# Kernel tuning notes

Hardware: AMD Instinct MI355X
Metric: run time of the kernel (lower is better)

The kernel has to match this reference:

```python
import jax, jax.numpy as jnp
import numpy as np

N = 100000       # nodes
E = 1600000      # edges (avg degree 16)
D_IN = 128
D_HID = 32
D_OUT = 32
H = 4            # heads
NEG_SLOPE = 0.2  # GATConv default leaky_relu slope


def setup_inputs() -> dict:
    key = jax.random.key(0)
    ks = jax.random.split(key, 10)
    s = 0.1
    return {
        "edge": jax.random.randint(ks[0], (2, E), 0, N),
        "features": jax.random.normal(ks[1], (N, D_IN), jnp.float32),
        # layer 1 params: W [in, H*hid], attention vectors per head [H, hid]
        "W1": jax.random.normal(ks[2], (D_IN, H * D_HID), jnp.float32) * s,
        "a1_src": jax.random.normal(ks[3], (H, D_HID), jnp.float32) * s,
        "a1_dst": jax.random.normal(ks[4], (H, D_HID), jnp.float32) * s,
        "b1": jnp.zeros((H * D_HID,), jnp.float32),
        # layer 2 params
        "W2": jax.random.normal(ks[5], (H * D_HID, H * D_OUT), jnp.float32) * s,
        "a2_src": jax.random.normal(ks[6], (H, D_OUT), jnp.float32) * s,
        "a2_dst": jax.random.normal(ks[7], (H, D_OUT), jnp.float32) * s,
        "b2": jnp.zeros((H * D_OUT,), jnp.float32),
    }


def gat_conv(x, src, dst, W, a_src, a_dst, b, heads, d_out):
    """Multi-head GAT layer, concat heads. x: [N, d_in] -> [N, heads*d_out]."""
    n = x.shape[0]
    h = (x @ W).reshape(n, heads, d_out)                 # [N,H,D]
    e_src = jnp.einsum('nhd,hd->nh', h, a_src)           # [N,H]
    e_dst = jnp.einsum('nhd,hd->nh', h, a_dst)           # [N,H]
    e = jax.nn.leaky_relu(e_src[src] + e_dst[dst], NEG_SLOPE)  # [E,H]
    # softmax over incoming edges of each dst node (stable via segment max)
    m = jax.lax.stop_gradient(jax.ops.segment_max(e, dst, num_segments=n))
    w = jnp.exp(e - m[dst])                              # [E,H]
    den = jax.ops.segment_sum(w, dst, num_segments=n)    # [N,H]
    alpha = w / den[dst]                                 # [E,H]
    out = jax.ops.segment_sum(alpha[:, :, None] * h[src], dst, num_segments=n)
    return out.reshape(n, heads * d_out) + b


def reference(edge, features, W1, a1_src, a1_dst, b1, W2, a2_src, a2_dst, b2):
    src, dst = edge[0], edge[1]
    h = jax.nn.relu(gat_conv(features, src, dst, W1, a1_src, a1_dst, b1, H, D_HID))
    h = gat_conv(h, src, dst, W2, a2_src, a2_dst, b2, H, D_OUT)
    return jax.nn.log_softmax(h, axis=1)
```

## Files before the change

kernel.cpp:

```cpp
#include <hip/hip_runtime.h>
#include <hip/hip_bf16.h>
#include <math.h>

#define N_NODES 100000
#define N_EDGES 1600000
#define NHEADS 4
#define NEG_SLOPE 0.2f
#define NB 1563
#define BCAP 2048

typedef __attribute__((ext_vector_type(8))) short short8;
typedef __attribute__((ext_vector_type(4))) float f32x4;

__device__ __forceinline__ unsigned short f2bf(float f) {
    unsigned int u = __float_as_uint(f);
    u += 0x7fffu + ((u >> 16) & 1u);
    return (unsigned short)(u >> 16);
}
__device__ __forceinline__ float bf_lo(unsigned int u) {
    return __uint_as_float(u << 16);
}
__device__ __forceinline__ float bf_hi(unsigned int u) {
    return __uint_as_float(u & 0xffff0000u);
}
__device__ __forceinline__ short8 pack8(float4 f0, float4 f1) {
    short8 v;
    v[0] = (short)f2bf(f0.x); v[1] = (short)f2bf(f0.y);
    v[2] = (short)f2bf(f0.z); v[3] = (short)f2bf(f0.w);
    v[4] = (short)f2bf(f1.x); v[5] = (short)f2bf(f1.y);
    v[6] = (short)f2bf(f1.z); v[7] = (short)f2bf(f1.w);
    return v;
}

__global__ void pack_w_kernel(const float* __restrict__ W,
                              const float* __restrict__ a_src,
                              const float* __restrict__ a_dst,
                              unsigned short* __restrict__ Wp) {
    int idx = blockIdx.x * 256 + threadIdx.x;
    if (idx >= 18432) return;
    int j    = idx & 7;
    int lane = (idx >> 3) & 63;
    int kc   = (idx >> 9) & 3;
    int ct   = idx >> 11;
    int k = kc * 32 + ((lane >> 4) & 3) * 8 + j;
    int n = lane & 15;
    float v = 0.f;
    if (ct < 8) {
        v = W[k * 128 + ct * 16 + n];
    } else if (n < 8) {
        int hd = n & 3;
        const float* av = (n < 4 ? a_src : a_dst) + hd * 32;
        const float* wr = W + k * 128 + hd * 32;
#pragma unroll
        for (int t = 0; t < 32; ++t) v = fmaf(wr[t], av[t], v);
    }
    Wp[idx] = f2bf(v);
}

template <bool XF32>
__global__ __launch_bounds__(256) void gemm_mfma_kernel(
        const void* __restrict__ xv,
        const unsigned short* __restrict__ Wp,
        unsigned short* __restrict__ h, float* __restrict__ esd, int n_rows) {
    __shared__ unsigned short Wl[18432];

    const int t = threadIdx.x;
    {
        const uint4* s4 = (const uint4*)Wp;
        uint4* d4 = (uint4*)Wl;
#pragma unroll
        for (int p = 0; p < 9; ++p) d4[p * 256 + t] = s4[p * 256 + t];
    }
    __syncthreads();

    const int lane = t & 63, wave = t >> 6;
    const int l15 = lane & 15, quad = lane >> 4;
    const int rbase = blockIdx.x * 128 + wave * 32;

    short8 a[2][4];
#pragma unroll
    for (int rt = 0; rt < 2; ++rt) {
        int r = rbase + rt * 16 + l15;
        r = r < n_rows ? r : n_rows - 1;
        if (XF32) {
            const float* xr = (const float*)xv + (size_t)r * 128 + quad * 8;
#pragma unroll
            for (int kc = 0; kc < 4; ++kc) {
                float4 f0 = *(const float4*)(xr + kc * 32);
                float4 f1 = *(const float4*)(xr + kc * 32 + 4);
                a[rt][kc] = pack8(f0, f1);
            }
        } else {
            const unsigned short* xr =
                (const unsigned short*)xv + (size_t)r * 128 + quad * 8;
#pragma unroll
            for (int kc = 0; kc < 4; ++kc)
                a[rt][kc] = *(const short8*)(xr + kc * 32);
        }
    }

    f32x4 acc[2][9];
#pragma unroll
    for (int rt = 0; rt < 2; ++rt)
#pragma unroll
        for (int ct = 0; ct < 9; ++ct)
            acc[rt][ct] = (f32x4){0.f, 0.f, 0.f, 0.f};

#pragma unroll
    for (int ct = 0; ct < 9; ++ct) {
#pragma unroll
        for (int kc = 0; kc < 4; ++kc) {
            short8 b = *(const short8*)&Wl[((ct * 4 + kc) * 64 + lane) * 8];
            acc[0][ct] = __builtin_amdgcn_mfma_f32_16x16x32_bf16(
                a[0][kc], b, acc[0][ct], 0, 0, 0);
            acc[1][ct] = __builtin_amdgcn_mfma_f32_16x16x32_bf16(
                a[1][kc], b, acc[1][ct], 0, 0, 0);
        }
    }

#pragma unroll
    for (int rt = 0; rt < 2; ++rt) {
#pragma unroll
        for (int i = 0; i < 4; ++i) {
            int r = rbase + rt * 16 + quad * 4 + i;
            if (r < n_rows) {
                unsigned short* hp = h + (size_t)r * 128 + l15;
#pragma unroll
                for (int ct = 0; ct < 8; ++ct)
                    hp[ct * 16] = f2bf(acc[rt][ct][i]);
                if (l15 < 8) esd[r * 8 + l15] = acc[rt][8][i];
            }
        }
    }
}

__global__ void zero_ints_kernel(int* __restrict__ p, int n) {
    int i = blockIdx.x * 256 + threadIdx.x;
    if (i < n) p[i] = 0;
}

__global__ void bucket_fill_kernel(const int* __restrict__ src,
                                   const int* __restrict__ dst,
                                   int* __restrict__ bcnt,
                                   unsigned int* __restrict__ slab) {
    int e = blockIdx.x * 256 + threadIdx.x;
    if (e >= N_EDGES) return;
    int d = dst[e];
    int b = d >> 6;
    int pos = atomicAdd(&bcnt[b * 16], 1);
    slab[(size_t)b * BCAP + pos] = (unsigned int)src[e] | ((unsigned int)(d & 63) << 17);
}

__global__ __launch_bounds__(256) void bucket_hist_kernel(
        const int* __restrict__ bcnt, const unsigned int* __restrict__ slab,
        int* __restrict__ deg) {
    __shared__ int hist[64];
    const int b = blockIdx.x;
    if (threadIdx.x < 64) hist[threadIdx.x] = 0;
    __syncthreads();
    const int m = bcnt[b * 16];
    const unsigned int* sp = slab + (size_t)b * BCAP;
    for (int i = threadIdx.x; i < m; i += 256)
        atomicAdd(&hist[sp[i] >> 17], 1);
    __syncthreads();
    if (threadIdx.x < 64) {
        int node = b * 64 + threadIdx.x;
        if (node < N_NODES) deg[node] = hist[threadIdx.x];
    }
}

__global__ __launch_bounds__(256) void scan1_kernel(const int* __restrict__ deg,
                                                    int* __restrict__ rowptr,
                                                    int* __restrict__ partials) {
    __shared__ int wsum[4];
    int i = blockIdx.x * 256 + threadIdx.x;
    int lane = threadIdx.x & 63, wave = threadIdx.x >> 6;
    int orig = (i < N_NODES) ? deg[i] : 0;
    int v = orig;
#pragma unroll
    for (int off = 1; off < 64; off <<= 1) {
        int t = __shfl_up(v, off);
        if (lane >= off) v += t;
    }
    if (lane == 63) wsum[wave] = v;
    __syncthreads();
    int woff = 0;
#pragma unroll
    for (int w = 0; w < 4; ++w) if (w < wave) woff += wsum[w];
    if (i < N_NODES) rowptr[i] = v - orig + woff;
    if (threadIdx.x == 0)
        partials[blockIdx.x] = wsum[0] + wsum[1] + wsum[2] + wsum[3];
}

__global__ __launch_bounds__(512) void scan2_kernel(int* __restrict__ partials,
                                                    int nb) {
    __shared__ int wsum[8];
    int i = threadIdx.x;
    int lane = i & 63, wave = i >> 6;
    int orig = (i < nb) ? partials[i] : 0;
    int v = orig;
#pragma unroll
    for (int off = 1; off < 64; off <<= 1) {
        int t = __shfl_up(v, off);
        if (lane >= off) v += t;
    }
    if (lane == 63) wsum[wave] = v;
    __syncthreads();
    int woff = 0;
#pragma unroll
    for (int w = 0; w < 8; ++w) if (w < wave) woff += wsum[w];
    if (i < nb) partials[i] = v - orig + woff;
}

__global__ void scan3_kernel(int* __restrict__ rowptr,
                             const int* __restrict__ partials) {
    int i = blockIdx.x * 256 + threadIdx.x;
    if (i < N_NODES) rowptr[i] += partials[blockIdx.x];
}

__global__ __launch_bounds__(256) void bucket_scatter_kernel(
        const int* __restrict__ bcnt, const unsigned int* __restrict__ slab,
        const int* __restrict__ rowptr, int* __restrict__ csr_src) {
    __shared__ int rp[64];
    __shared__ int cnt[64];
    const int b = blockIdx.x;
    if (threadIdx.x < 64) {
        int node = b * 64 + threadIdx.x;
        rp[threadIdx.x] = node < N_NODES ? rowptr[node] : 0;
        cnt[threadIdx.x] = 0;
    }
    __syncthreads();
    const int m = bcnt[b * 16];
    const unsigned int* sp = slab + (size_t)b * BCAP;
    for (int i = threadIdx.x; i < m; i += 256) {
        unsigned int rec = sp[i];
        int local = rec >> 17;
        int pos = rp[local] + atomicAdd(&cnt[local], 1);
        csr_src[pos] = (int)(rec & 0x1FFFFu);
    }
}

template <bool LOGSOFTMAX>
__global__ __launch_bounds__(256) void aggregate_kernel(
        const int* __restrict__ csr_src, const int* __restrict__ rowptr,
        const int* __restrict__ deg, const float* __restrict__ esd,
        const unsigned short* __restrict__ hb, const float* __restrict__ b,
        void* __restrict__ out) {
    const int lane = threadIdx.x & 63;
    const int wave = threadIdx.x >> 6;
    const int n = blockIdx.x * 4 + wave;
    if (n >= N_NODES) return;
    const int eo = lane >> 4;
    const int cl = lane & 15;
    const int c0 = cl * 8;
    const int hd = cl >> 2;
    const float edn = esd[n * 8 + 4 + hd];
    const int base = rowptr[n];
    const int dg = deg[n];

    float acc[8] = {0.f, 0.f, 0.f, 0.f, 0.f, 0.f, 0.f, 0.f};
    float wsum = 0.f;

    if (dg > 0) {
        const int myidx = csr_src[base + (lane < dg ? lane : dg - 1)];
        const int nit = (dg + 3) >> 2;

        auto getS = [&](int j) -> int {
            int o = 4 * j + eo;
            if (4 * j < 64) return __shfl(myidx, o);
            int oc = o < dg ? o : dg - 1;
            return csr_src[base + oc];
        };
        auto loadP = [&](int s) -> uint4 {
            return *(const uint4*)(hb + (size_t)s * 128 + c0);
        };

        int s0 = getS(0);
        uint4 p0 = loadP(s0);
        float e0 = esd[s0 * 8 + hd];
        uint4 p1 = p0; float e1 = e0;
        if (nit > 1) {
            int s1 = getS(1);
            p1 = loadP(s1);
            e1 = esd[s1 * 8 + hd];
        }
        for (int j = 0; j < nit; ++j) {
            uint4 p2 = p1; float e2 = e1;
            if (j + 2 < nit) {
                int s2 = getS(j + 2);
                p2 = loadP(s2);
                e2 = esd[s2 * 8 + hd];
            }
            int o = 4 * j + eo;
            float sc = e0 + edn;
            sc = sc > 0.f ? sc : NEG_SLOPE * sc;
            float w = (o < dg) ? __expf(sc) : 0.f;
            acc[0] = fmaf(w, bf_lo(p0.x), acc[0]);
            acc[1] = fmaf(w, bf_hi(p0.x), acc[1]);
            acc[2] = fmaf(w, bf_lo(p0.y), acc[2]);
            acc[3] = fmaf(w, bf_hi(p0.y), acc[3]);
            acc[4] = fmaf(w, bf_lo(p0.z), acc[4]);
            acc[5] = fmaf(w, bf_hi(p0.z), acc[5]);
            acc[6] = fmaf(w, bf_lo(p0.w), acc[6]);
            acc[7] = fmaf(w, bf_hi(p0.w), acc[7]);
            wsum += w;
            p0 = p1; e0 = e1; p1 = p2; e1 = e2;
        }
    }

#pragma unroll
    for (int j = 0; j < 8; ++j) {
        acc[j] += __shfl_xor(acc[j], 16);
        acc[j] += __shfl_xor(acc[j], 32);
    }
    wsum += __shfl_xor(wsum, 16);
    wsum += __shfl_xor(wsum, 32);

    float inv = wsum > 0.f ? 1.f / wsum : 0.f;
    float bl[8];
    *(float4*)&bl[0] = *(const float4*)(b + c0);
    *(float4*)&bl[4] = *(const float4*)(b + c0 + 4);
    float v[8];
#pragma unroll
    for (int j = 0; j < 8; ++j) v[j] = acc[j] * inv + bl[j];

    if (!LOGSOFTMAX) {
        if (lane < 16) {
            unsigned int pk[4];
#pragma unroll
            for (int j = 0; j < 4; ++j) {
                float r0 = v[2 * j]     > 0.f ? v[2 * j]     : 0.f;
                float r1 = v[2 * j + 1] > 0.f ? v[2 * j + 1] : 0.f;
                pk[j] = (unsigned int)f2bf(r0) | ((unsigned int)f2bf(r1) << 16);
            }
            *(uint4*)((unsigned short*)out + (size_t)n * 128 + c0) =
                make_uint4(pk[0], pk[1], pk[2], pk[3]);
        }
    } else {
        float m = v[0];
#pragma unroll
        for (int j = 1; j < 8; ++j) m = fmaxf(m, v[j]);
#pragma unroll
        for (int s = 1; s < 16; s <<= 1) m = fmaxf(m, __shfl_xor(m, s));
        float se = 0.f;
#pragma unroll
        for (int j = 0; j < 8; ++j) se += __expf(v[j] - m);
#pragma unroll
        for (int s = 1; s < 16; s <<= 1) se += __shfl_xor(se, s);
        float ls = m + logf(se);
        if (lane < 16) {
            float* o = (float*)out + (size_t)n * 128 + c0;
            *(float4*)o = make_float4(v[0] - ls, v[1] - ls, v[2] - ls, v[3] - ls);
            *(float4*)(o + 4) = make_float4(v[4] - ls, v[5] - ls, v[6] - ls, v[7] - ls);
        }
    }
}

extern "C" void kernel_launch(void* const* d_in, const int* in_sizes, int n_in,
                              void* d_out, int out_size, void* d_ws, size_t ws_size,
                              hipStream_t stream) {
    const int*   edge = (const int*)d_in[0];
    const int*   src  = edge;
    const int*   dst  = edge + N_EDGES;
    const float* feat = (const float*)d_in[1];
    const float* W1   = (const float*)d_in[2];
    const float* a1s  = (const float*)d_in[3];
    const float* a1d  = (const float*)d_in[4];
    const float* b1   = (const float*)d_in[5];
    const float* W2   = (const float*)d_in[6];
    const float* a2s  = (const float*)d_in[7];
    const float* a2d  = (const float*)d_in[8];
    const float* b2   = (const float*)d_in[9];
    float* out = (float*)d_out;

    unsigned short* hb  = (unsigned short*)d_ws;
    unsigned short* x1b = hb + (size_t)N_NODES * 128;
    unsigned short* Wp1 = x1b + (size_t)N_NODES * 128;
    unsigned short* Wp2 = Wp1 + 18432;
    float* esd = (float*)(Wp2 + 18432);
    int* deg      = (int*)(esd + (size_t)N_NODES * 8);
    int* rowptr   = deg + N_NODES;
    int* partials = rowptr + N_NODES;
    int* bcnt     = partials + 512;
    unsigned int* slab = (unsigned int*)(bcnt + NB * 16);
    int* csr_src  = (int*)(slab + (size_t)NB * BCAP);

    const int node_blk  = (N_NODES + 255) / 256;
    const int edge_blk  = (N_EDGES + 255) / 256;
    const int gemm_blk  = (N_NODES + 127) / 128;
    const int agg_blk   = (N_NODES + 3) / 4;

    zero_ints_kernel<<<(NB * 16 + 255) / 256, 256, 0, stream>>>(bcnt, NB * 16);
    bucket_fill_kernel<<<edge_blk, 256, 0, stream>>>(src, dst, bcnt, slab);
    bucket_hist_kernel<<<NB, 256, 0, stream>>>(bcnt, slab, deg);
    scan1_kernel<<<node_blk, 256, 0, stream>>>(deg, rowptr, partials);
    scan2_kernel<<<1, 512, 0, stream>>>(partials, node_blk);
    scan3_kernel<<<node_blk, 256, 0, stream>>>(rowptr, partials);
    bucket_scatter_kernel<<<NB, 256, 0, stream>>>(bcnt, slab, rowptr, csr_src);

    pack_w_kernel<<<72, 256, 0, stream>>>(W1, a1s, a1d, Wp1);
    pack_w_kernel<<<72, 256, 0, stream>>>(W2, a2s, a2d, Wp2);

    gemm_mfma_kernel<true><<<gemm_blk, 256, 0, stream>>>(feat, Wp1, hb, esd, N_NODES);
    aggregate_kernel<false><<<agg_blk, 256, 0, stream>>>(
        csr_src, rowptr, deg, esd, hb, b1, x1b);

    gemm_mfma_kernel<false><<<gemm_blk, 256, 0, stream>>>(x1b, Wp2, hb, esd, N_NODES);
    aggregate_kernel<true><<<agg_blk, 256, 0, stream>>>(
        csr_src, rowptr, deg, esd, hb, b2, out);
}
```

Baseline: 401.9 us.

## Two-level binning for CSR build and batched gathers in aggregation

Replaces per-edge global atomics into 1563 small buckets with a block-local shared-memory binning into 49 coarse buckets split into 8 sub-slabs, flushed to global memory in 16-element chunks. Histogram and scatter then work on 2048-node buckets with larger shared arrays. The aggregate kernel issues up to 8 neighbour row loads up front instead of a depth-2 software pipeline. It also splits the src and dst attention scores into separate arrays so each source score is loaded by one lane and shuffled to the others. The trade-offs are fixed capacities (SUBCAP, BUKCAP) that could overflow on skewed degree distributions, and higher register use in aggregation.

After: 410.7 us. 1.02x slower.

```diff
diff --git a/kernel.cpp b/kernel.cpp
--- a/kernel.cpp
+++ b/kernel.cpp
@@ -6,8 +6,9 @@
 #define N_EDGES 1600000
 #define NHEADS 4
 #define NEG_SLOPE 0.2f
-#define NB 1563
-#define BCAP 2048
+#define NBUK 49
+#define BUKCAP 272
+#define SUBCAP 4608
 
 typedef __attribute__((ext_vector_type(8))) short short8;
 typedef __attribute__((ext_vector_type(4))) float f32x4;
@@ -61,7 +62,8 @@
 __global__ __launch_bounds__(256) void gemm_mfma_kernel(
         const void* __restrict__ xv,
         const unsigned short* __restrict__ Wp,
-        unsigned short* __restrict__ h, float* __restrict__ esd, int n_rows) {
+        unsigned short* __restrict__ h,
+        float* __restrict__ es, float* __restrict__ ed, int n_rows) {
     __shared__ unsigned short Wl[18432];
 
     const int t = threadIdx.x;
@@ -128,7 +130,8 @@
 #pragma unroll
                 for (int ct = 0; ct < 8; ++ct)
                     hp[ct * 16] = f2bf(acc[rt][ct][i]);
-                if (l15 < 8) esd[r * 8 + l15] = acc[rt][8][i];
+                if (l15 < 4)      es[r * 4 + l15]       = acc[rt][8][i];
+                else if (l15 < 8) ed[r * 4 + (l15 - 4)] = acc[rt][8][i];
             }
         }
     }
@@ -139,33 +142,75 @@
     if (i < n) p[i] = 0;
 }
 
-__global__ void bucket_fill_kernel(const int* __restrict__ src,
-                                   const int* __restrict__ dst,
-                                   int* __restrict__ bcnt,
-                                   unsigned int* __restrict__ slab) {
-    int e = blockIdx.x * 256 + threadIdx.x;
-    if (e >= N_EDGES) return;
-    int d = dst[e];
-    int b = d >> 6;
-    int pos = atomicAdd(&bcnt[b * 16], 1);
-    slab[(size_t)b * BCAP + pos] = (unsigned int)src[e] | ((unsigned int)(d & 63) << 17);
-}
-
-__global__ __launch_bounds__(256) void bucket_hist_kernel(
-        const int* __restrict__ bcnt, const unsigned int* __restrict__ slab,
+__global__ __launch_bounds__(256) void bin_fill_kernel(
+        const int* __restrict__ src, const int* __restrict__ dst,
+        int* __restrict__ gcnt, unsigned int* __restrict__ slab) {
+    __shared__ unsigned int lbuf[NBUK * BUKCAP];
+    __shared__ int cnt[NBUK];
+    const int t = threadIdx.x;
+    const int sub = blockIdx.x & 7;
+    if (t < NBUK) cnt[t] = 0;
+    __syncthreads();
+
+    const int per = (N_EDGES + gridDim.x - 1) / gridDim.x;
+    const int e0 = blockIdx.x * per;
+    const int e1 = (e0 + per < N_EDGES) ? e0 + per : N_EDGES;
+
+    for (int eb = e0; eb < e1; eb += 256) {
+        int e = eb + t;
+        if (e < e1) {
+            int d = dst[e];
+            int s = src[e];
+            int bk = d >> 11;
+            int pos = atomicAdd(&cnt[bk], 1);
+            lbuf[bk * BUKCAP + pos] =
+                (unsigned int)s | ((unsigned int)(d & 2047) << 17);
+        }
+        __syncthreads();
+        if (t < NBUK) {
+            int pending = cnt[t];
+            int nl = pending >> 4;
+            if (nl > 0) {
+                int gpos = atomicAdd(&gcnt[(t * 8 + sub) * 16], nl * 16);
+                unsigned int* gp =
+                    slab + (size_t)(t * 8 + sub) * SUBCAP + gpos;
+                for (int l = 0; l < nl * 16; l += 4)
+                    *(uint4*)(gp + l) = *(uint4*)&lbuf[t * BUKCAP + l];
+                int rem = pending & 15;
+                for (int r2 = 0; r2 < rem; ++r2)
+                    lbuf[t * BUKCAP + r2] = lbuf[t * BUKCAP + nl * 16 + r2];
+                cnt[t] = rem;
+            }
+        }
+        __syncthreads();
+    }
+    if (t < NBUK) {
+        int rem = cnt[t];
+        if (rem > 0) {
+            int gpos = atomicAdd(&gcnt[(t * 8 + sub) * 16], rem);
+            unsigned int* gp = slab + (size_t)(t * 8 + sub) * SUBCAP + gpos;
+            for (int r2 = 0; r2 < rem; ++r2) gp[r2] = lbuf[t * BUKCAP + r2];
+        }
+    }
+}
+
+__global__ __launch_bounds__(256) void bin_hist_kernel(
+        const int* __restrict__ gcnt, const unsigned int* __restrict__ slab,
         int* __restrict__ deg) {
-    __shared__ int hist[64];
+    __shared__ int hist[2048];
+    const int t = threadIdx.x;
     const int b = blockIdx.x;
-    if (threadIdx.x < 64) hist[threadIdx.x] = 0;
-    __syncthreads();
-    const int m = bcnt[b * 16];
-    const unsigned int* sp = slab + (size_t)b * BCAP;
-    for (int i = threadIdx.x; i < m; i += 256)
-        atomicAdd(&hist[sp[i] >> 17], 1);
-    __syncthreads();
-    if (threadIdx.x < 64) {
-        int node = b * 64 + threadIdx.x;
-        if (node < N_NODES) deg[node] = hist[threadIdx.x];
+    for (int i = t; i < 2048; i += 256) hist[i] = 0;
+    __syncthreads();
+    for (int sub = 0; sub < 8; ++sub) {
+        int m = gcnt[(b * 8 + sub) * 16];
+        const unsigned int* sp = slab + (size_t)(b * 8 + sub) * SUBCAP;
+        for (int i = t; i < m; i += 256) atomicAdd(&hist[sp[i] >> 17], 1);
+    }
+    __syncthreads();
+    for (int i = t; i < 2048; i += 256) {
+        int node = b * 2048 + i;
+        if (node < N_NODES) deg[node] = hist[i];
     }
 }
 
@@ -218,32 +263,36 @@
     if (i < N_NODES) rowptr[i] += partials[blockIdx.x];
 }
 
-__global__ __launch_bounds__(256) void bucket_scatter_kernel(
-        const int* __restrict__ bcnt, const unsigned int* __restrict__ slab,
+__global__ __launch_bounds__(256) void bin_scatter_kernel(
+        const int* __restrict__ gcnt, const unsigned int* __restrict__ slab,
         const int* __restrict__ rowptr, int* __restrict__ csr_src) {
-    __shared__ int rp[64];
-    __shared__ int cnt[64];
+    __shared__ int rp[2048];
+    __shared__ int c2[2048];
+    const int t = threadIdx.x;
     const int b = blockIdx.x;
-    if (threadIdx.x < 64) {
-        int node = b * 64 + threadIdx.x;
-        rp[threadIdx.x] = node < N_NODES ? rowptr[node] : 0;
-        cnt[threadIdx.x] = 0;
-    }
-    __syncthreads();
-    const int m = bcnt[b * 16];
-    const unsigned int* sp = slab + (size_t)b * BCAP;
-    for (int i = threadIdx.x; i < m; i += 256) {
-        unsigned int rec = sp[i];
-        int local = rec >> 17;
-        int pos = rp[local] + atomicAdd(&cnt[local], 1);
-        csr_src[pos] = (int)(rec & 0x1FFFFu);
+    for (int i = t; i < 2048; i += 256) {
+        int node = b * 2048 + i;
+        rp[i] = node < N_NODES ? rowptr[node] : 0;
+        c2[i] = 0;
+    }
+    __syncthreads();
+    for (int sub = 0; sub < 8; ++sub) {
+        int m = gcnt[(b * 8 + sub) * 16];
+        const unsigned int* sp = slab + (size_t)(b * 8 + sub) * SUBCAP;
+        for (int i = t; i < m; i += 256) {
+            unsigned int rec = sp[i];
+            int local = rec >> 17;
+            int pos = rp[local] + atomicAdd(&c2[local], 1);
+            csr_src[pos] = (int)(rec & 0x1FFFFu);
+        }
     }
 }
 
 template <bool LOGSOFTMAX>
 __global__ __launch_bounds__(256) void aggregate_kernel(
         const int* __restrict__ csr_src, const int* __restrict__ rowptr,
-        const int* __restrict__ deg, const float* __restrict__ esd,
+        const int* __restrict__ deg,
+        const float* __restrict__ es, const float* __restrict__ ed,
         const unsigned short* __restrict__ hb, const float* __restrict__ b,
         void* __restrict__ out) {
     const int lane = threadIdx.x & 63;
@@ -254,7 +303,7 @@
     const int cl = lane & 15;
     const int c0 = cl * 8;
     const int hd = cl >> 2;
-    const float edn = esd[n * 8 + 4 + hd];
+    const float edn = ed[n * 4 + hd];
     const int base = rowptr[n];
     const int dg = deg[n];
 
@@ -264,47 +313,55 @@
     if (dg > 0) {
         const int myidx = csr_src[base + (lane < dg ? lane : dg - 1)];
         const int nit = (dg + 3) >> 2;
-
-        auto getS = [&](int j) -> int {
+        const int nf = nit < 8 ? nit : 8;
+
+        uint4 P[8];
+        float E[8];
+#pragma unroll
+        for (int j = 0; j < 8; ++j) {
+            if (j < nf) {
+                int s = __shfl(myidx, 4 * j + eo);
+                P[j] = *(const uint4*)(hb + (size_t)s * 128 + c0);
+                E[j] = (cl < 4) ? es[s * 4 + cl] : 0.f;
+            }
+        }
+#pragma unroll
+        for (int j = 0; j < 8; ++j) {
+            if (j < nf) {
+                float e = __shfl(E[j], (lane & 48) | (cl >> 2));
+                int o = 4 * j + eo;
+                float sc = e + edn;
+                sc = sc > 0.f ? sc : NEG_SLOPE * sc;
+                float w = (o < dg) ? __expf(sc) : 0.f;
+                acc[0] = fmaf(w, bf_lo(P[j].x), acc[0]);
+                acc[1] = fmaf(w, bf_hi(P[j].x), acc[1]);
+                acc[2] = fmaf(w, bf_lo(P[j].y), acc[2]);
+                acc[3] = fmaf(w, bf_hi(P[j].y), acc[3]);
+                acc[4] = fmaf(w, bf_lo(P[j].z), acc[4]);
+                acc[5] = fmaf(w, bf_hi(P[j].z), acc[5]);
+                acc[6] = fmaf(w, bf_lo(P[j].w), acc[6]);
+                acc[7] = fmaf(w, bf_hi(P[j].w), acc[7]);
+                wsum += w;
+            }
+        }
+        for (int j = 8; j < nit; ++j) {
             int o = 4 * j + eo;
-            if (4 * j < 64) return __shfl(myidx, o);
-            int oc = o < dg ? o : dg - 1;
-            return csr_src[base + oc];
-        };
-        auto loadP = [&](int s) -> uint4 {
-            return *(const uint4*)(hb + (size_t)s * 128 + c0);
-        };
-
-        int s0 = getS(0);
-        uint4 p0 = loadP(s0);
-        float e0 = esd[s0 * 8 + hd];
-        uint4 p1 = p0; float e1 = e0;
-        if (nit > 1) {
-            int s1 = getS(1);
-            p1 = loadP(s1);
-            e1 = esd[s1 * 8 + hd];
-        }
-        for (int j = 0; j < nit; ++j) {
-            uint4 p2 = p1; float e2 = e1;
-            if (j + 2 < nit) {
-                int s2 = getS(j + 2);
-                p2 = loadP(s2);
-                e2 = esd[s2 * 8 + hd];
-            }
-            int o = 4 * j + eo;
-            float sc = e0 + edn;
+            int s = (o < 64) ? __shfl(myidx, o)
+                             : csr_src[base + (o < dg ? o : dg - 1)];
+            uint4 p = *(const uint4*)(hb + (size_t)s * 128 + c0);
+            float e = es[s * 4 + hd];
+            float sc = e + edn;
             sc = sc > 0.f ? sc : NEG_SLOPE * sc;
             float w = (o < dg) ? __expf(sc) : 0.f;
-            acc[0] = fmaf(w, bf_lo(p0.x), acc[0]);
-            acc[1] = fmaf(w, bf_hi(p0.x), acc[1]);
-            acc[2] = fmaf(w, bf_lo(p0.y), acc[2]);
-            acc[3] = fmaf(w, bf_hi(p0.y), acc[3]);
-            acc[4] = fmaf(w, bf_lo(p0.z), acc[4]);
-            acc[5] = fmaf(w, bf_hi(p0.z), acc[5]);
-            acc[6] = fmaf(w, bf_lo(p0.w), acc[6]);
-            acc[7] = fmaf(w, bf_hi(p0.w), acc[7]);
+            acc[0] = fmaf(w, bf_lo(p.x), acc[0]);
+            acc[1] = fmaf(w, bf_hi(p.x), acc[1]);
+            acc[2] = fmaf(w, bf_lo(p.y), acc[2]);
+            acc[3] = fmaf(w, bf_hi(p.y), acc[3]);
+            acc[4] = fmaf(w, bf_lo(p.z), acc[4]);
+            acc[5] = fmaf(w, bf_hi(p.z), acc[5]);
+            acc[6] = fmaf(w, bf_lo(p.w), acc[6]);
+            acc[7] = fmaf(w, bf_hi(p.w), acc[7]);
             wsum += w;
-            p0 = p1; e0 = e1; p1 = p2; e1 = e2;
         }
     }
 
@@ -377,35 +434,35 @@
     unsigned short* x1b = hb + (size_t)N_NODES * 128;
     unsigned short* Wp1 = x1b + (size_t)N_NODES * 128;
     unsigned short* Wp2 = Wp1 + 18432;
-    float* esd = (float*)(Wp2 + 18432);
-    int* deg      = (int*)(esd + (size_t)N_NODES * 8);
+    float* es = (float*)(Wp2 + 18432);
+    float* ed = es + (size_t)N_NODES * 4;
+    int* deg      = (int*)(ed + (size_t)N_NODES * 4);
     int* rowptr   = deg + N_NODES;
     int* partials = rowptr + N_NODES;
-    int* bcnt     = partials + 512;
-    unsigned int* slab = (unsigned int*)(bcnt + NB * 16);
-    int* csr_src  = (int*)(slab + (size_t)NB * BCAP);
-
-    const int node_blk  = (N_NODES + 255) / 256;
-    const int edge_blk  = (N_EDGES + 255) / 256;
-    const int gemm_blk  = (N_NODES + 127) / 128;
-    const int agg_blk   = (N_NODES + 3) / 4;
-
-    zero_ints_kernel<<<(NB * 16 + 255) / 256, 256, 0, stream>>>(bcnt, NB * 16);
-    bucket_fill_kernel<<<edge_blk, 256, 0, stream>>>(src, dst, bcnt, slab);
-    bucket_hist_kernel<<<NB, 256, 0, stream>>>(bcnt, slab, deg);
+    int* gcnt     = partials + 512;
+    unsigned int* slab = (unsigned int*)(gcnt + NBUK * 8 * 16);
+    int* csr_src  = (int*)(slab + (size_t)NBUK * 8 * SUBCAP);
+
+    const int node_blk = (N_NODES + 255) / 256;
+    const int gemm_blk = (N_NODES + 127) / 128;
+    const int agg_blk  = (N_NODES + 3) / 4;
+
+    zero_ints_kernel<<<(NBUK * 8 * 16 + 255) / 256, 256, 0, stream>>>(gcnt, NBUK * 8 * 16);
+    bin_fill_kernel<<<256, 256, 0, stream>>>(src, dst, gcnt, slab);
+    bin_hist_kernel<<<NBUK, 256, 0, stream>>>(gcnt, slab, deg);
     scan1_kernel<<<node_blk, 256, 0, stream>>>(deg, rowptr, partials);
     scan2_kernel<<<1, 512, 0, stream>>>(partials, node_blk);
     scan3_kernel<<<node_blk, 256, 0, stream>>>(rowptr, partials);
-    bucket_scatter_kernel<<<NB, 256, 0, stream>>>(bcnt, slab, rowptr, csr_src);
+    bin_scatter_kernel<<<NBUK, 256, 0, stream>>>(gcnt, slab, rowptr, csr_src);
 
     pack_w_kernel<<<72, 256, 0, stream>>>(W1, a1s, a1d, Wp1);
     pack_w_kernel<<<72, 256, 0, stream>>>(W2, a2s, a2d, Wp2);
 
-    gemm_mfma_kernel<true><<<gemm_blk, 256, 0, stream>>>(feat, Wp1, hb, esd, N_NODES);
+    gemm_mfma_kernel<true><<<gemm_blk, 256, 0, stream>>>(feat, Wp1, hb, es, ed, N_NODES);
     aggregate_kernel<false><<<agg_blk, 256, 0, stream>>>(
-        csr_src, rowptr, deg, esd, hb, b1, x1b);
-
-    gemm_mfma_kernel<false><<<gemm_blk, 256, 0, stream>>>(x1b, Wp2, hb, esd, N_NODES);
+        csr_src, rowptr, deg, es, ed, hb, b1, x1b);
+
+    gemm_mfma_kernel<false><<<gemm_blk, 256, 0, stream>>>(x1b, Wp2, hb, es, ed, N_NODES);
     aggregate_kernel<true><<<agg_blk, 256, 0, stream>>>(
-        csr_src, rowptr, deg, esd, hb, b2, out);
-}
+        csr_src, rowptr, deg, es, ed, hb, b2, out);
+}
```
